# Optimization experiments

Measured on AMD Instinct MI355X. Metric: run time of the kernel, lower is better.

## Reference

```python
import jax, jax.numpy as jnp
import numpy as np

B, LC, LT = 2, 1024, 1024
DS, DF = 2, 1
EOBS = 4                 # nn.Embed(2, 4)
D_IN = EOBS + DS + DF    # concat(obs, s, f)
EMB_H, D = 256, 64       # embed_obs_s_f = MLP([256, 64])
H, DH = 8, 8             # heads x head_dim = D
FFN_H = 128              # ffn = MLP([128, 64])
BIAS_H = 16              # DistanceBias hidden width
HEAD_H = 128             # head = MLP([128, 2])
NBLK = 6                 # num_blks (num_reps = 1)
EPS = 1e-6

def _ln(x, scale, bias):
    mu = jnp.mean(x, -1, keepdims=True)
    var = jnp.var(x, -1, keepdims=True)
    return (x - mu) * jax.lax.rsqrt(var + EPS) * scale + bias

def _mlp(x, w1, b1, w2, b2):
    return jax.nn.relu(x @ w1 + b1) @ w2 + b2

def _dist_bias(d, w1, b1, w2, b2):
    # d: [B, Lq, Lk] scalar distances -> per-head bias [B, H, Lq, Lk]
    h = jax.nn.relu(d[..., None] @ w1 + b1)
    return jnp.transpose(h @ w2 + b2, (0, 3, 1, 2))

def _mha(q_in, kv_in, wq, bq, wk, bk, wv, bv, wo, bo, bias):
    q = (q_in @ wq + bq).reshape(*q_in.shape[:-1], H, DH)
    k = (kv_in @ wk + bk).reshape(*kv_in.shape[:-1], H, DH)
    v = (kv_in @ wv + bv).reshape(*kv_in.shape[:-1], H, DH)
    scores = jnp.einsum('bqhd,bkhd->bhqk', q, k) / np.sqrt(DH).astype(np.float32) + bias
    a = jax.nn.softmax(scores, axis=-1)
    o = jnp.einsum('bhqk,bkhd->bqhd', a, v).reshape(*q_in.shape[:-1], D)
    return o @ wo + bo

def _forward(s_ctx, f_ctx, s_test, embed_obs_table, emb_w1, emb_b1, emb_w2, emb_b2,
             attn_wq, attn_bq, attn_wk, attn_bk, attn_wv, attn_bv, attn_wo, attn_bo,
             ffn_w1, ffn_b1, ffn_w2, ffn_b2, bias_w1, bias_b1, bias_w2, bias_b2,
             norm_scale, norm_bias, fnorm_scale, fnorm_bias,
             head_w1, head_b1, head_w2, head_b2):
    Bv, Lt = s_test.shape[0], s_test.shape[1]
    f_test = jnp.zeros((Bv, Lt, f_ctx.shape[-1]), f_ctx.dtype)
    obs = jnp.broadcast_to(embed_obs_table[1], (*f_ctx.shape[:-1], EOBS))
    unobs = jnp.broadcast_to(embed_obs_table[0], (Bv, Lt, EOBS))
    kvs = _mlp(jnp.concatenate([obs, s_ctx, f_ctx], -1), emb_w1, emb_b1, emb_w2, emb_b2)
    qvs = _mlp(jnp.concatenate([unobs, s_test, f_test], -1), emb_w1, emb_b1, emb_w2, emb_b2)
    # vmap(l2_dist_sq): pairwise squared L2 distances per batch element
    d_qk = jnp.sum((s_test[:, :, None, :] - s_ctx[:, None, :, :]) ** 2, -1)
    d_kk = jnp.sum((s_ctx[:, :, None, :] - s_ctx[:, None, :, :]) ** 2, -1)
    for i in range(NBLK):
        b_qk = _dist_bias(d_qk, bias_w1[i], bias_b1[i], bias_w2[i], bias_b2[i])
        b_kk = _dist_bias(d_kk, bias_w1[i], bias_b1[i], bias_w2[i], bias_b2[i])
        aw = (attn_wq[i], attn_bq[i], attn_wk[i], attn_bk[i], attn_wv[i], attn_bv[i], attn_wo[i], attn_bo[i])
        ns, nb = norm_scale[i], norm_bias[i]
        q_att = _ln(qvs + _mha(qvs, kvs, *aw, b_qk), ns, nb)
        k_att = _ln(kvs + _mha(kvs, kvs, *aw, b_kk), ns, nb)
        qvs = _ln(q_att + _mlp(q_att, ffn_w1[i], ffn_b1[i], ffn_w2[i], ffn_b2[i]), ns, nb)
        kvs = _ln(k_att + _mlp(k_att, ffn_w1[i], ffn_b1[i], ffn_w2[i], ffn_b2[i]), ns, nb)
    qvs = _ln(qvs, fnorm_scale, fnorm_bias)
    f_dist = _mlp(qvs, head_w1, head_b1, head_w2, head_b2)
    f_mu, f_log_var = jnp.split(f_dist, 2, axis=-1)
    f_std = jnp.exp(f_log_var / 2)  # min_std = 0.0
    return f_mu, f_std

def setup_inputs() -> dict:
    key = jax.random.key(0)
    ks = iter(jax.random.split(key, 40))
    r = lambda shp, s=0.05: jax.random.normal(next(ks), shp, jnp.float32) * s
    return dict(
        s_ctx=r((B, LC, DS), 1.0), f_ctx=r((B, LC, DF), 1.0), s_test=r((B, LT, DS), 1.0),
        embed_obs_table=r((2, EOBS)),
        emb_w1=r((D_IN, EMB_H)), emb_b1=jnp.zeros((EMB_H,)),
        emb_w2=r((EMB_H, D)), emb_b2=jnp.zeros((D,)),
        attn_wq=r((NBLK, D, D)), attn_bq=jnp.zeros((NBLK, D)),
        attn_wk=r((NBLK, D, D)), attn_bk=jnp.zeros((NBLK, D)),
        attn_wv=r((NBLK, D, D)), attn_bv=jnp.zeros((NBLK, D)),
        attn_wo=r((NBLK, D, D)), attn_bo=jnp.zeros((NBLK, D)),
        ffn_w1=r((NBLK, D, FFN_H)), ffn_b1=jnp.zeros((NBLK, FFN_H)),
        ffn_w2=r((NBLK, FFN_H, D)), ffn_b2=jnp.zeros((NBLK, D)),
        bias_w1=r((NBLK, 1, BIAS_H)), bias_b1=jnp.zeros((NBLK, BIAS_H)),
        bias_w2=r((NBLK, BIAS_H, H)), bias_b2=jnp.zeros((NBLK, H)),
        norm_scale=jnp.ones((NBLK, D)), norm_bias=jnp.zeros((NBLK, D)),
        fnorm_scale=jnp.ones((D,)), fnorm_bias=jnp.zeros((D,)),
        head_w1=r((D, HEAD_H)), head_b1=jnp.zeros((HEAD_H,)),
        head_w2=r((HEAD_H, 2)), head_b2=jnp.zeros((2,)),
    )

def reference(s_ctx, f_ctx, s_test, embed_obs_table, emb_w1, emb_b1, emb_w2, emb_b2,
              attn_wq, attn_bq, attn_wk, attn_bk, attn_wv, attn_bv, attn_wo, attn_bo,
              ffn_w1, ffn_b1, ffn_w2, ffn_b2, bias_w1, bias_b1, bias_w2, bias_b2,
              norm_scale, norm_bias, fnorm_scale, fnorm_bias,
              head_w1, head_b1, head_w2, head_b2):
    return _forward(s_ctx, f_ctx, s_test, embed_obs_table, emb_w1, emb_b1, emb_w2, emb_b2,
                    attn_wq, attn_bq, attn_wk, attn_bk, attn_wv, attn_bv, attn_wo, attn_bo,
                    ffn_w1, ffn_b1, ffn_w2, ffn_b2, bias_w1, bias_b1, bias_w2, bias_b2,
                    norm_scale, norm_bias, fnorm_scale, fnorm_bias,
                    head_w1, head_b1, head_w2, head_b2)
```

## Files before the change

kernel.cpp:

```cpp
#include <hip/hip_runtime.h>
#include <hip/hip_bf16.h>

typedef __hip_bfloat16 bf16;
typedef float v2f __attribute__((ext_vector_type(2)));

#define LEN 1024
#define N2 2048
#define SCALE_L2E 0.5100697918f

#define I_SCTX   0
#define I_FCTX   4096
#define I_STEST  6144
#define I_OBS    10240
#define I_EW1    10248
#define I_EB1    12040
#define I_EW2    12296
#define I_EB2    28680
#define I_WQ     28744
#define I_BQ     53320
#define I_WK     53704
#define I_BK     78280
#define I_WV     78664
#define I_BV     103240
#define I_WO     103624
#define I_BO     128200
#define I_FW1    128584
#define I_FB1    177736
#define I_FW2    178504
#define I_FB2    227656
#define I_BW1    228040
#define I_BB1    228136
#define I_BW2    228232
#define I_BB2    229000
#define I_NS     229048
#define I_NB     229432
#define I_FNS    229816
#define I_FNB    229880
#define I_HW1    229944
#define I_HB1    238136
#define I_HW2    238264
#define I_HB2    238520

#define OFF_PW   240256
#define OFF_QVS  262144
#define OFF_KVS  393216
#define OFF_Q1   524288
#define OFF_Q2   655360
#define OFF_KB   786432
#define OFF_VB   917504
#define OFF_PART 1048576
#define PART_KS  196608

__constant__ int C_OFFS[33] = {
    0, 4096, 6144, 10240, 10248, 12040, 12296, 28680, 28744, 53320, 53704,
    78280, 78664, 103240, 103624, 128200, 128584, 177736, 178504, 227656,
    228040, 228136, 228232, 229000, 229048, 229432, 229816, 229880, 229944,
    238136, 238264, 238520, 238522 };

struct InPtrs { const void* p[32]; };

__device__ __forceinline__ float pack2(float a, float b) {
    __hip_bfloat16 ha = __float2bfloat16(a), hb = __float2bfloat16(b);
    unsigned ua = *(unsigned short*)&ha, ub = *(unsigned short*)&hb;
    return __uint_as_float(ua | (ub << 16));
}
__device__ __forceinline__ float unlo(float f) {
    return __uint_as_float(__float_as_uint(f) << 16);
}
__device__ __forceinline__ float unhi(float f) {
    return __uint_as_float(__float_as_uint(f) & 0xffff0000u);
}

__global__ __launch_bounds__(256) void k_cvt(InPtrs ptrs, float* ws) {
    const unsigned u0 = *(const unsigned*)ptrs.p[24];
    const int isbf = (u0 == 0x3F803F80u);
    const int i = blockIdx.y;
    const int o0 = C_OFFS[i], n = C_OFFS[i + 1] - o0;
    const void* src = ptrs.p[i];
    for (int j = blockIdx.x * 256 + threadIdx.x; j < n; j += gridDim.x * 256) {
        float v = isbf ? __bfloat162float(((const bf16*)src)[j])
                       : ((const float*)src)[j];
        ws[o0 + j] = v;
    }
}

__global__ __launch_bounds__(256) void k_pw(float* ws) {
    const int L = blockIdx.x, t = threadIdx.x;
    __shared__ float w1s[16], b1s[16], bps[16];
    __shared__ int rnk[16];
    if (t < 16) {
        float w = ws[I_BW1 + L * 16 + t], b0 = ws[I_BB1 + L * 16 + t];
        w1s[t] = w; b1s[t] = b0;
        bps[t] = (w != 0.f) ? (-b0 / w) : 1e30f;
    }
    __syncthreads();
    if (t < 16) {
        float me = bps[t]; int r = 0;
        for (int j = 0; j < 16; ++j) {
            float o = bps[j];
            if (o < me || (o == me && j < t)) ++r;
        }
        rnk[t] = r;
    }
    __syncthreads();
    if (t < 16) ws[OFF_PW + L * 288 + 272 + rnk[t]] = bps[t];
    if (t < 136) {
        int s = t >> 3, h = t & 7;
        float slope = 0.f, inter = ws[I_BB2 + L * 8 + h];
        for (int j = 0; j < 16; ++j) {
            float w = w1s[j];
            bool act = (w > 0.f) ? (rnk[j] < s)
                     : (w < 0.f) ? (rnk[j] >= s)
                                 : (b1s[j] > 0.f);
            if (act) {
                float w2v = ws[I_BW2 + L * 128 + j * 8 + h];
                slope += w * w2v;
                inter += b1s[j] * w2v;
            }
        }
        const float LOG2E = 1.4426950408889634f;
        ws[OFF_PW + L * 288 + (s * 8 + h) * 2]     = slope * LOG2E;
        ws[OFF_PW + L * 288 + (s * 8 + h) * 2 + 1] = inter * LOG2E;
    }
}

__global__ __launch_bounds__(256) void k_embed(float* ws) {
    __shared__ float hbuf[256];
    __shared__ float red[256];
    int r = blockIdx.x, t = threadIdx.x;
    bool is_ctx = (r < N2);
    int rr = is_ctx ? r : r - N2;
    const float* ob = ws + I_OBS + (is_ctx ? 4 : 0);
    const float* s  = ws + (is_ctx ? I_SCTX : I_STEST);
    float in[7];
    in[0] = ob[0]; in[1] = ob[1]; in[2] = ob[2]; in[3] = ob[3];
    in[4] = s[rr * 2]; in[5] = s[rr * 2 + 1];
    in[6] = is_ctx ? ws[I_FCTX + rr] : 0.f;

    float acc = ws[I_EB1 + t];
#pragma unroll
    for (int i = 0; i < 7; ++i) acc += in[i] * ws[I_EW1 + i * 256 + t];
    hbuf[t] = fmaxf(acc, 0.f);
    __syncthreads();

    int d = t & 63, p = t >> 6;
    float a2 = 0.f;
#pragma unroll 8
    for (int j = p * 64; j < p * 64 + 64; ++j) a2 += hbuf[j] * ws[I_EW2 + j * 64 + d];
    red[t] = a2;
    __syncthreads();
    if (t < 64) {
        float o = red[t] + red[64 + t] + red[128 + t] + red[192 + t] + ws[I_EB2 + t];
        float* dst = ws + (is_ctx ? OFF_KVS : OFF_QVS);
        dst[rr * 64 + t] = o;
    }
}

__global__ __launch_bounds__(256) void k_qkv(int blk, float* ws) {
    __shared__ float xs[2][64];
    int r = blockIdx.x, t = threadIdx.x;
    if (t < 64)       xs[0][t] = ws[OFF_QVS + r * 64 + t];
    else if (t < 128) xs[1][t - 64] = ws[OFF_KVS + r * 64 + (t - 64)];
    __syncthreads();
    int o = t >> 6, d = t & 63;
    const float* x = (o == 0) ? xs[0] : xs[1];
    const float* W; const float* bb; float* dst;
    if (o <= 1)      { W = ws + I_WQ + blk * 4096; bb = ws + I_BQ + blk * 64; dst = ws + (o == 0 ? OFF_Q1 : OFF_Q2); }
    else if (o == 2) { W = ws + I_WK + blk * 4096; bb = ws + I_BK + blk * 64; dst = ws + OFF_KB; }
    else             { W = ws + I_WV + blk * 4096; bb = ws + I_BV + blk * 64; dst = ws + OFF_VB; }
    float acc = bb[d];
#pragma unroll 8
    for (int k = 0; k < 64; ++k) acc += x[k] * W[k * 64 + d];
    dst[r * 64 + d] = acc;
}

__global__ __launch_bounds__(256, 4) void k_attn(int blk, float* ws) {
    __shared__ float Ks[2176];
    __shared__ float Vs[2176];
    __shared__ float Sds[544];
    __shared__ v2f   pw[136];

    const int t = threadIdx.x;
    const int qt = blockIdx.x, ks = blockIdx.y, z = blockIdx.z;
    const int b = z & 1, kind = z >> 1;
    const int q0 = qt * 16;
    const float* Qbuf = ws + (kind == 0 ? OFF_Q1 : OFF_Q2);
    const float* Kbuf = ws + OFF_KB;
    const float* Vbuf = ws + OFF_VB;
    const float* sq_src = ws + (kind == 0 ? I_STEST : I_SCTX);
    const float* sk_src = ws + I_SCTX;
    const float* pwg = ws + OFF_PW + blk * 288;

    float bp[16];
#pragma unroll
    for (int j = 0; j < 16; ++j) bp[j] = pwg[272 + j];

    if (t < 136) pw[t] = (v2f){ pwg[t * 2], pwg[t * 2 + 1] };

    const int par = t & 7, h2 = (t >> 3) & 7, q4 = t >> 6;
    const int pq = t >> 4, pk = t & 15;
    float sqx, sqy;
    {
        const float* sp = sq_src + (b * LEN + q0 + pq) * 2;
        sqx = sp[0]; sqy = sp[1];
    }

    v2f qf[4][4];
#pragma unroll
    for (int i = 0; i < 4; ++i) {
        const float* qp = Qbuf + (b * LEN + q0 + q4 + 4 * i) * 64 + h2 * 8;
        float4 qa = *(const float4*)qp;
        float4 qb = *(const float4*)(qp + 4);
        qf[i][0] = (v2f){qa.x, qa.y}; qf[i][1] = (v2f){qa.z, qa.w};
        qf[i][2] = (v2f){qb.x, qb.y}; qf[i][3] = (v2f){qb.z, qb.w};
    }

    float m[4] = {-1e30f, -1e30f, -1e30f, -1e30f};
    float l[4] = {};
    v2f oacc[4][4] = {};

    for (int kt = ks * 4; kt < ks * 4 + 4; ++kt) {
        __syncthreads();
        {
            int kr = t >> 3, j = (t & 7) * 8;
            const float* ksrc = Kbuf + (b * LEN + kt * 32 + kr) * 64 + j;
            const float* vsrc = Vbuf + (b * LEN + kt * 32 + kr) * 64 + j;
            *(float4*)&Ks[kr * 68 + j]     = *(const float4*)ksrc;
            *(float4*)&Ks[kr * 68 + j + 4] = *(const float4*)(ksrc + 4);
            *(float4*)&Vs[kr * 68 + j]     = *(const float4*)vsrc;
            *(float4*)&Vs[kr * 68 + j + 4] = *(const float4*)(vsrc + 4);
        }
        {
            float4 kc = *(const float4*)(sk_src + (b * LEN + kt * 32 + pk * 2) * 2);
            float dx0 = sqx - kc.x, dy0 = sqy - kc.y;
            float dx1 = sqx - kc.z, dy1 = sqy - kc.w;
            float d0 = dx0 * dx0 + dy0 * dy0;
            float d1 = dx1 * dx1 + dy1 * dy1;
            int s0 = 0, s1 = 0;
#pragma unroll
            for (int j = 0; j < 16; ++j) { s0 += (d0 > bp[j]); s1 += (d1 > bp[j]); }
            Sds[(pk * 2) * 17 + pq]     = __uint_as_float((__float_as_uint(d0) & ~31u) | s0);
            Sds[(pk * 2 + 1) * 17 + pq] = __uint_as_float((__float_as_uint(d1) & ~31u) | s1);
        }
        __syncthreads();

        float sv[16];
#pragma unroll
        for (int j = 0; j < 4; ++j) {
            int k = par + 8 * j;
            const v2f* kf = (const v2f*)&Ks[k * 68 + h2 * 8];
            v2f k0 = kf[0], k1 = kf[1], k2 = kf[2], k3 = kf[3];
#pragma unroll
            for (int i = 0; i < 4; ++i) {
                unsigned u = __float_as_uint(Sds[k * 17 + q4 + 4 * i]);
                float dv = __uint_as_float(u & ~31u);
                v2f pv_ = pw[(u & 31u) * 8 + h2];
                v2f acc = qf[i][0] * k0;
                acc += qf[i][1] * k1;
                acc += qf[i][2] * k2;
                acc += qf[i][3] * k3;
                sv[i * 4 + j] = (acc.x + acc.y) * SCALE_L2E + (pv_.x * dv + pv_.y);
            }
        }
#pragma unroll
        for (int i = 0; i < 4; ++i) {
            float tm = m[i];
#pragma unroll
            for (int j = 0; j < 4; ++j) tm = fmaxf(tm, sv[i * 4 + j]);
            float alpha = exp2f(m[i] - tm);
            l[i] *= alpha;
            v2f av = (v2f){alpha, alpha};
#pragma unroll
            for (int c = 0; c < 4; ++c) oacc[i][c] *= av;
            m[i] = tm;
#pragma unroll
            for (int j = 0; j < 4; ++j) {
                float p = exp2f(sv[i * 4 + j] - tm);
                sv[i * 4 + j] = p;
                l[i] += p;
            }
        }
#pragma unroll
        for (int j = 0; j < 4; ++j) {
            int k = par + 8 * j;
            const v2f* vf = (const v2f*)&Vs[k * 68 + h2 * 8];
            v2f v0 = vf[0], v1 = vf[1], v2 = vf[2], v3 = vf[3];
#pragma unroll
            for (int i = 0; i < 4; ++i) {
                float p = sv[i * 4 + j];
                v2f pp = (v2f){p, p};
                oacc[i][0] += pp * v0;
                oacc[i][1] += pp * v1;
                oacc[i][2] += pp * v2;
                oacc[i][3] += pp * v3;
            }
        }
    }

#pragma unroll
    for (int st = 1; st <= 4; st <<= 1) {
#pragma unroll
        for (int i = 0; i < 4; ++i) {
            float mo = __shfl_xor(m[i], st);
            float Mx = fmaxf(m[i], mo);
            float a0 = exp2f(m[i] - Mx), a1 = exp2f(mo - Mx);
            float lo = __shfl_xor(l[i], st);
            l[i] = l[i] * a0 + lo * a1;
#pragma unroll
            for (int c = 0; c < 4; ++c) {
                v2f x = oacc[i][c];
                float x0 = x.x * a0 + __shfl_xor(x.x, st) * a1;
                float x1 = x.y * a0 + __shfl_xor(x.y, st) * a1;
                oacc[i][c] = (v2f){x0, x1};
            }
            m[i] = Mx;
        }
    }

    __syncthreads();
    float* stg = Ks;
    if (par == 0) {
#pragma unroll
        for (int i = 0; i < 4; ++i) {
            float inv = 1.f / l[i];
            float lse = m[i] + log2f(l[i]);
            float* p = &stg[(q4 + 4 * i) * 48 + h2 * 6];
            p[0] = pack2(oacc[i][0].x * inv, oacc[i][0].y * inv);
            p[1] = pack2(oacc[i][1].x * inv, oacc[i][1].y * inv);
            p[2] = pack2(oacc[i][2].x * inv, oacc[i][2].y * inv);
            p[3] = pack2(oacc[i][3].x * inv, oacc[i][3].y * inv);
            p[4] = lse; p[5] = 0.f;
        }
    }
    __syncthreads();
    if (t < 192) {
        float* dst = ws + OFF_PART + ks * PART_KS + (z * LEN + q0) * 48;
        *(float4*)(dst + t * 4) = *(const float4*)(stg + t * 4);
    }
}

__global__ __launch_bounds__(128) void k_fuse(int blk, float* ws, const void* ns_raw, void* out_raw) {
    __shared__ float xo[4 * 68];
    __shared__ float xsm[4 * 68];
    __shared__ float hs[4 * 132];
    __shared__ float xn[4 * 68];
    const int t = threadIdx.x;
    const int kind = blockIdx.y;
    const int r0 = blockIdx.x * 4;
    float* io = ws + (kind == 0 ? OFF_QVS : OFF_KVS);

    {
        int r = t >> 5, h = (t >> 2) & 7, q = t & 3;
        int rg = r0 + r, b = rg >> 10, row = rg & 1023, z = kind * 2 + b;
        const float* e0 = ws + OFF_PART + q * PART_KS + ((z * LEN + row) * 8 + h) * 6;
        const float* e1 = e0 + 4 * PART_KS;
        v2f a0 = *(const v2f*)e0, a1 = *(const v2f*)(e0 + 2), a2 = *(const v2f*)(e0 + 4);
        v2f c0 = *(const v2f*)e1, c1 = *(const v2f*)(e1 + 2), c2 = *(const v2f*)(e1 + 4);
        float M = fmaxf(a2.x, c2.x);
        M = fmaxf(M, __shfl_xor(M, 1));
        M = fmaxf(M, __shfl_xor(M, 2));
        float wA = exp2f(a2.x - M), wB = exp2f(c2.x - M);
        float den = wA + wB;
        float num[8];
        num[0] = wA * unlo(a0.x) + wB * unlo(c0.x);
        num[1] = wA * unhi(a0.x) + wB * unhi(c0.x);
        num[2] = wA * unlo(a0.y) + wB * unlo(c0.y);
        num[3] = wA * unhi(a0.y) + wB * unhi(c0.y);
        num[4] = wA * unlo(a1.x) + wB * unlo(c1.x);
        num[5] = wA * unhi(a1.x) + wB * unhi(c1.x);
        num[6] = wA * unlo(a1.y) + wB * unlo(c1.y);
        num[7] = wA * unhi(a1.y) + wB * unhi(c1.y);
        den += __shfl_xor(den, 1); den += __shfl_xor(den, 2);
#pragma unroll
        for (int d_ = 0; d_ < 8; ++d_) {
            num[d_] += __shfl_xor(num[d_], 1);
            num[d_] += __shfl_xor(num[d_], 2);
        }
        float invd = 1.f / den;
        xo[r * 68 + h * 8 + 2 * q]     = num[2 * q] * invd;
        xo[r * 68 + h * 8 + 2 * q + 1] = num[2 * q + 1] * invd;
    }
    __syncthreads();

    const int r = t >> 5, dd = (t & 31) * 2;
    const int rg = r0 + r;
    float xs0, xs1;

    {
        const float* Wo = ws + I_WO + blk * 4096;
        v2f acc = *(const v2f*)(ws + I_BO + blk * 64 + dd);
#pragma unroll 8
        for (int k = 0; k < 64; ++k) {
            float xv = xo[r * 68 + k];
            v2f w = *(const v2f*)(Wo + k * 64 + dd);
            acc.x += xv * w.x; acc.y += xv * w.y;
        }
        v2f rv = *(const v2f*)(io + rg * 64 + dd);
        acc.x += rv.x; acc.y += rv.y;
        float s = acc.x + acc.y, s2 = acc.x * acc.x + acc.y * acc.y;
#pragma unroll
        for (int off = 1; off < 32; off <<= 1) { s += __shfl_xor(s, off); s2 += __shfl_xor(s2, off); }
        float mu = s * (1.f / 64.f);
        float var = s2 * (1.f / 64.f) - mu * mu;
        float rs = rsqrtf(fmaxf(var, 0.f) + 1e-6f);
        v2f nsv = *(const v2f*)(ws + I_NS + blk * 64 + dd);
        v2f nbv = *(const v2f*)(ws + I_NB + blk * 64 + dd);
        xs0 = (acc.x - mu) * rs * nsv.x + nbv.x;
        xs1 = (acc.y - mu) * rs * nsv.y + nbv.y;
        *(v2f*)&xsm[r * 68 + dd] = (v2f){xs0, xs1};
    }
    __syncthreads();

    {
        int rc = t >> 5, c4 = (t & 31) * 4;
        const float* W1 = ws + I_FW1 + blk * 8192;
        float4 acc = *(const float4*)(ws + I_FB1 + blk * 128 + c4);
#pragma unroll 4
        for (int k = 0; k < 64; ++k) {
            float xv = xsm[rc * 68 + k];
            float4 w = *(const float4*)(W1 + k * 128 + c4);
            acc.x += xv * w.x; acc.y += xv * w.y; acc.z += xv * w.z; acc.w += xv * w.w;
        }
        acc.x = fmaxf(acc.x, 0.f); acc.y = fmaxf(acc.y, 0.f);
        acc.z = fmaxf(acc.z, 0.f); acc.w = fmaxf(acc.w, 0.f);
        *(float4*)&hs[rc * 132 + c4] = acc;
    }
    __syncthreads();

    float v0, v1;
    {
        const float* W2 = ws + I_FW2 + blk * 8192;
        v2f acc = *(const v2f*)(ws + I_FB2 + blk * 64 + dd);
#pragma unroll 8
        for (int k = 0; k < 128; ++k) {
            float hv = hs[r * 132 + k];
            v2f w = *(const v2f*)(W2 + k * 64 + dd);
            acc.x += hv * w.x; acc.y += hv * w.y;
        }
        acc.x += xs0; acc.y += xs1;
        float s = acc.x + acc.y, s2 = acc.x * acc.x + acc.y * acc.y;
#pragma unroll
        for (int off = 1; off < 32; off <<= 1) { s += __shfl_xor(s, off); s2 += __shfl_xor(s2, off); }
        float mu = s * (1.f / 64.f);
        float var = s2 * (1.f / 64.f) - mu * mu;
        float rs = rsqrtf(fmaxf(var, 0.f) + 1e-6f);
        v2f nsv = *(const v2f*)(ws + I_NS + blk * 64 + dd);
        v2f nbv = *(const v2f*)(ws + I_NB + blk * 64 + dd);
        v0 = (acc.x - mu) * rs * nsv.x + nbv.x;
        v1 = (acc.y - mu) * rs * nsv.y + nbv.y;
        *(v2f*)(io + rg * 64 + dd) = (v2f){v0, v1};
        *(v2f*)&xn[r * 68 + dd] = (v2f){v0, v1};
    }
    __syncthreads();

    if (blk < 5) {
        const int nb_ = blk + 1;
        if (kind == 0) {
            const float* WQ = ws + I_WQ + nb_ * 4096;
            v2f acc = *(const v2f*)(ws + I_BQ + nb_ * 64 + dd);
#pragma unroll 8
            for (int k = 0; k < 64; ++k) {
                float xv = xn[r * 68 + k];
                v2f w = *(const v2f*)(WQ + k * 64 + dd);
                acc.x += xv * w.x; acc.y += xv * w.y;
            }
            *(v2f*)(ws + OFF_Q1 + rg * 64 + dd) = acc;
        } else {
            const float* WQ = ws + I_WQ + nb_ * 4096;
            const float* WK = ws + I_WK + nb_ * 4096;
            const float* WV = ws + I_WV + nb_ * 4096;
            v2f aq = *(const v2f*)(ws + I_BQ + nb_ * 64 + dd);
            v2f ak = *(const v2f*)(ws + I_BK + nb_ * 64 + dd);
            v2f av = *(const v2f*)(ws + I_BV + nb_ * 64 + dd);
#pragma unroll 4
            for (int k = 0; k < 64; ++k) {
                float xv = xn[r * 68 + k];
                v2f wq = *(const v2f*)(WQ + k * 64 + dd);
                v2f wk = *(const v2f*)(WK + k * 64 + dd);
                v2f wv = *(const v2f*)(WV + k * 64 + dd);
                aq.x += xv * wq.x; aq.y += xv * wq.y;
                ak.x += xv * wk.x; ak.y += xv * wk.y;
                av.x += xv * wv.x; av.y += xv * wv.y;
            }
            *(v2f*)(ws + OFF_Q2 + rg * 64 + dd) = aq;
            *(v2f*)(ws + OFF_KB + rg * 64 + dd) = ak;
            *(v2f*)(ws + OFF_VB + rg * 64 + dd) = av;
        }
    } else if (kind == 0) {
        {
            float s = v0 + v1, s2 = v0 * v0 + v1 * v1;
#pragma unroll
            for (int off = 1; off < 32; off <<= 1) { s += __shfl_xor(s, off); s2 += __shfl_xor(s2, off); }
            float mu = s * (1.f / 64.f);
            float var = s2 * (1.f / 64.f) - mu * mu;
            float rs = rsqrtf(fmaxf(var, 0.f) + 1e-6f);
            v2f fns = *(const v2f*)(ws + I_FNS + dd);
            v2f fnb = *(const v2f*)(ws + I_FNB + dd);
            *(v2f*)&xsm[r * 68 + dd] = (v2f){ (v0 - mu) * rs * fns.x + fnb.x,
                                              (v1 - mu) * rs * fns.y + fnb.y };
        }
        __syncthreads();
        {
            int rc = t >> 5, c4 = (t & 31) * 4;
            const float* W1 = ws + I_HW1;
            float4 acc = *(const float4*)(ws + I_HB1 + c4);
#pragma unroll 4
            for (int k = 0; k < 64; ++k) {
                float xv = xsm[rc * 68 + k];
                float4 w = *(const float4*)(W1 + k * 128 + c4);
                acc.x += xv * w.x; acc.y += xv * w.y; acc.z += xv * w.z; acc.w += xv * w.w;
            }
            acc.x = fmaxf(acc.x, 0.f); acc.y = fmaxf(acc.y, 0.f);
            acc.z = fmaxf(acc.z, 0.f); acc.w = fmaxf(acc.w, 0.f);
            *(float4*)&hs[rc * 132 + c4] = acc;
        }
        __syncthreads();
        if (t < 8) {
            int rr = t >> 1, c = t & 1;
            float a = ws[I_HB2 + c];
            for (int k = 0; k < 128; ++k) a += hs[rr * 132 + k] * ws[I_HW2 + k * 2 + c];
            float v = c ? exp2f(a * 0.7213475204444817f) : a;
            int rgg = r0 + rr;
            int idx = c ? (N2 + rgg) : rgg;
            unsigned u0 = *(const unsigned*)ns_raw;
            if (u0 == 0x3F803F80u) ((bf16*)out_raw)[idx] = __float2bfloat16(v);
            else                   ((float*)out_raw)[idx] = v;
        }
    }
}

extern "C" void kernel_launch(void* const* d_in, const int* in_sizes, int n_in,
                              void* d_out, int out_size, void* d_ws, size_t ws_size,
                              hipStream_t stream) {
    float* ws = (float*)d_ws;

    InPtrs ptrs;
    for (int i = 0; i < 32; ++i) ptrs.p[i] = d_in[i];

    k_cvt<<<dim3(8, 32), 256, 0, stream>>>(ptrs, ws);
    k_pw<<<6, 256, 0, stream>>>(ws);
    k_embed<<<4096, 256, 0, stream>>>(ws);
    k_qkv<<<2048, 256, 0, stream>>>(0, ws);
    for (int i = 0; i < 6; ++i) {
        k_attn<<<dim3(64, 8, 4), 256, 0, stream>>>(i, ws);
        k_fuse<<<dim3(512, 2), 128, 0, stream>>>(i, ws, d_in[24], d_out);
    }
}
```

Measured before the change: 634.3 us.

## Shrink attention per-thread tiles, write partials directly, and split fuse into 2-row blocks

k_attn now gives each thread 2 query rows and 8 keys instead of 4 rows and 4 keys, which cuts register use so launch bounds can rise to 7 waves per SIMD. Partial outputs go straight to global memory in a per-row, per-head layout, removing the shared-memory staging and its barrier. k_fuse becomes a 64-thread block handling 2 rows, with twice as many blocks, and merges all 8 key-split partials per head inside one thread instead of shuffling. The trade-offs are more scattered small global writes from attention, more softmax merge steps per output, and more redundant weight reads across the smaller fuse blocks.

```diff
diff --git a/kernel.cpp b/kernel.cpp
--- a/kernel.cpp
+++ b/kernel.cpp
@@ -49,7 +49,6 @@
 #define OFF_KB   786432
 #define OFF_VB   917504
 #define OFF_PART 1048576
-#define PART_KS  196608
 
 __constant__ int C_OFFS[33] = {
     0, 4096, 6144, 10240, 10248, 12040, 12296, 28680, 28744, 53320, 53704,
@@ -174,7 +173,7 @@
     dst[r * 64 + d] = acc;
 }
 
-__global__ __launch_bounds__(256, 4) void k_attn(int blk, float* ws) {
+__global__ __launch_bounds__(256, 7) void k_attn(int blk, float* ws) {
     __shared__ float Ks[2176];
     __shared__ float Vs[2176];
     __shared__ float Sds[544];
@@ -197,7 +196,7 @@
 
     if (t < 136) pw[t] = (v2f){ pwg[t * 2], pwg[t * 2 + 1] };
 
-    const int par = t & 7, h2 = (t >> 3) & 7, q4 = t >> 6;
+    const int q2 = t >> 5, h2 = (t >> 2) & 7, par = t & 3;
     const int pq = t >> 4, pk = t & 15;
     float sqx, sqy;
     {
@@ -205,19 +204,19 @@
         sqx = sp[0]; sqy = sp[1];
     }
 
-    v2f qf[4][4];
-#pragma unroll
-    for (int i = 0; i < 4; ++i) {
-        const float* qp = Qbuf + (b * LEN + q0 + q4 + 4 * i) * 64 + h2 * 8;
+    v2f qf[2][4];
+#pragma unroll
+    for (int i = 0; i < 2; ++i) {
+        const float* qp = Qbuf + (b * LEN + q0 + q2 + 8 * i) * 64 + h2 * 8;
         float4 qa = *(const float4*)qp;
         float4 qb = *(const float4*)(qp + 4);
         qf[i][0] = (v2f){qa.x, qa.y}; qf[i][1] = (v2f){qa.z, qa.w};
         qf[i][2] = (v2f){qb.x, qb.y}; qf[i][3] = (v2f){qb.z, qb.w};
     }
 
-    float m[4] = {-1e30f, -1e30f, -1e30f, -1e30f};
-    float l[4] = {};
-    v2f oacc[4][4] = {};
+    float m[2] = {-1e30f, -1e30f};
+    float l[2] = {};
+    v2f oacc[2][4] = {};
 
     for (int kt = ks * 4; kt < ks * 4 + 4; ++kt) {
         __syncthreads();
@@ -244,29 +243,29 @@
         }
         __syncthreads();
 
-        float sv[16];
-#pragma unroll
-        for (int j = 0; j < 4; ++j) {
-            int k = par + 8 * j;
+        float sv[2][8];
+#pragma unroll
+        for (int j = 0; j < 8; ++j) {
+            int k = par + 4 * j;
             const v2f* kf = (const v2f*)&Ks[k * 68 + h2 * 8];
             v2f k0 = kf[0], k1 = kf[1], k2 = kf[2], k3 = kf[3];
 #pragma unroll
-            for (int i = 0; i < 4; ++i) {
-                unsigned u = __float_as_uint(Sds[k * 17 + q4 + 4 * i]);
+            for (int i = 0; i < 2; ++i) {
+                unsigned u = __float_as_uint(Sds[k * 17 + q2 + 8 * i]);
                 float dv = __uint_as_float(u & ~31u);
                 v2f pv_ = pw[(u & 31u) * 8 + h2];
                 v2f acc = qf[i][0] * k0;
                 acc += qf[i][1] * k1;
                 acc += qf[i][2] * k2;
                 acc += qf[i][3] * k3;
-                sv[i * 4 + j] = (acc.x + acc.y) * SCALE_L2E + (pv_.x * dv + pv_.y);
-            }
-        }
-#pragma unroll
-        for (int i = 0; i < 4; ++i) {
+                sv[i][j] = (acc.x + acc.y) * SCALE_L2E + (pv_.x * dv + pv_.y);
+            }
+        }
+#pragma unroll
+        for (int i = 0; i < 2; ++i) {
             float tm = m[i];
 #pragma unroll
-            for (int j = 0; j < 4; ++j) tm = fmaxf(tm, sv[i * 4 + j]);
+            for (int j = 0; j < 8; ++j) tm = fmaxf(tm, sv[i][j]);
             float alpha = exp2f(m[i] - tm);
             l[i] *= alpha;
             v2f av = (v2f){alpha, alpha};
@@ -274,20 +273,20 @@
             for (int c = 0; c < 4; ++c) oacc[i][c] *= av;
             m[i] = tm;
 #pragma unroll
-            for (int j = 0; j < 4; ++j) {
-                float p = exp2f(sv[i * 4 + j] - tm);
-                sv[i * 4 + j] = p;
+            for (int j = 0; j < 8; ++j) {
+                float p = exp2f(sv[i][j] - tm);
+                sv[i][j] = p;
                 l[i] += p;
             }
         }
 #pragma unroll
-        for (int j = 0; j < 4; ++j) {
-            int k = par + 8 * j;
+        for (int j = 0; j < 8; ++j) {
+            int k = par + 4 * j;
             const v2f* vf = (const v2f*)&Vs[k * 68 + h2 * 8];
             v2f v0 = vf[0], v1 = vf[1], v2 = vf[2], v3 = vf[3];
 #pragma unroll
-            for (int i = 0; i < 4; ++i) {
-                float p = sv[i * 4 + j];
+            for (int i = 0; i < 2; ++i) {
+                float p = sv[i][j];
                 v2f pp = (v2f){p, p};
                 oacc[i][0] += pp * v0;
                 oacc[i][1] += pp * v1;
@@ -298,9 +297,9 @@
     }
 
 #pragma unroll
-    for (int st = 1; st <= 4; st <<= 1) {
-#pragma unroll
-        for (int i = 0; i < 4; ++i) {
+    for (int st = 1; st <= 2; st <<= 1) {
+#pragma unroll
+        for (int i = 0; i < 2; ++i) {
             float mo = __shfl_xor(m[i], st);
             float Mx = fmaxf(m[i], mo);
             float a0 = exp2f(m[i] - Mx), a1 = exp2f(mo - Mx);
@@ -317,139 +316,131 @@
         }
     }
 
-    __syncthreads();
-    float* stg = Ks;
     if (par == 0) {
 #pragma unroll
-        for (int i = 0; i < 4; ++i) {
+        for (int i = 0; i < 2; ++i) {
             float inv = 1.f / l[i];
             float lse = m[i] + log2f(l[i]);
-            float* p = &stg[(q4 + 4 * i) * 48 + h2 * 6];
-            p[0] = pack2(oacc[i][0].x * inv, oacc[i][0].y * inv);
-            p[1] = pack2(oacc[i][1].x * inv, oacc[i][1].y * inv);
-            p[2] = pack2(oacc[i][2].x * inv, oacc[i][2].y * inv);
-            p[3] = pack2(oacc[i][3].x * inv, oacc[i][3].y * inv);
-            p[4] = lse; p[5] = 0.f;
-        }
-    }
-    __syncthreads();
-    if (t < 192) {
-        float* dst = ws + OFF_PART + ks * PART_KS + (z * LEN + q0) * 48;
-        *(float4*)(dst + t * 4) = *(const float4*)(stg + t * 4);
-    }
-}
-
-__global__ __launch_bounds__(128) void k_fuse(int blk, float* ws, const void* ns_raw, void* out_raw) {
-    __shared__ float xo[4 * 68];
-    __shared__ float xsm[4 * 68];
-    __shared__ float hs[4 * 132];
-    __shared__ float xn[4 * 68];
+            int row = q0 + q2 + 8 * i;
+            float* p = ws + OFF_PART + (z * LEN + row) * 384 + h2 * 48 + ks * 6;
+            *(v2f*)(p)     = (v2f){ pack2(oacc[i][0].x * inv, oacc[i][0].y * inv),
+                                    pack2(oacc[i][1].x * inv, oacc[i][1].y * inv) };
+            *(v2f*)(p + 2) = (v2f){ pack2(oacc[i][2].x * inv, oacc[i][2].y * inv),
+                                    pack2(oacc[i][3].x * inv, oacc[i][3].y * inv) };
+            *(v2f*)(p + 4) = (v2f){ lse, 0.f };
+        }
+    }
+}
+
+__global__ __launch_bounds__(64) void k_fuse(int blk, float* ws, const void* ns_raw, void* out_raw) {
+    __shared__ float xo[2][64];
+    __shared__ float xsm[2][64];
+    __shared__ float hs[2][128];
+    __shared__ float xn[2][64];
     const int t = threadIdx.x;
     const int kind = blockIdx.y;
-    const int r0 = blockIdx.x * 4;
+    const int g = blockIdx.x;
+    const int rg0 = g * 2, rg1 = g * 2 + 1;
     float* io = ws + (kind == 0 ? OFF_QVS : OFF_KVS);
 
     {
-        int r = t >> 5, h = (t >> 2) & 7, q = t & 3;
-        int rg = r0 + r, b = rg >> 10, row = rg & 1023, z = kind * 2 + b;
-        const float* e0 = ws + OFF_PART + q * PART_KS + ((z * LEN + row) * 8 + h) * 6;
-        const float* e1 = e0 + 4 * PART_KS;
-        v2f a0 = *(const v2f*)e0, a1 = *(const v2f*)(e0 + 2), a2 = *(const v2f*)(e0 + 4);
-        v2f c0 = *(const v2f*)e1, c1 = *(const v2f*)(e1 + 2), c2 = *(const v2f*)(e1 + 4);
-        float M = fmaxf(a2.x, c2.x);
-        M = fmaxf(M, __shfl_xor(M, 1));
-        M = fmaxf(M, __shfl_xor(M, 2));
-        float wA = exp2f(a2.x - M), wB = exp2f(c2.x - M);
-        float den = wA + wB;
-        float num[8];
-        num[0] = wA * unlo(a0.x) + wB * unlo(c0.x);
-        num[1] = wA * unhi(a0.x) + wB * unhi(c0.x);
-        num[2] = wA * unlo(a0.y) + wB * unlo(c0.y);
-        num[3] = wA * unhi(a0.y) + wB * unhi(c0.y);
-        num[4] = wA * unlo(a1.x) + wB * unlo(c1.x);
-        num[5] = wA * unhi(a1.x) + wB * unhi(c1.x);
-        num[6] = wA * unlo(a1.y) + wB * unlo(c1.y);
-        num[7] = wA * unhi(a1.y) + wB * unhi(c1.y);
-        den += __shfl_xor(den, 1); den += __shfl_xor(den, 2);
-#pragma unroll
-        for (int d_ = 0; d_ < 8; ++d_) {
-            num[d_] += __shfl_xor(num[d_], 1);
-            num[d_] += __shfl_xor(num[d_], 2);
-        }
-        float invd = 1.f / den;
-        xo[r * 68 + h * 8 + 2 * q]     = num[2 * q] * invd;
-        xo[r * 68 + h * 8 + 2 * q + 1] = num[2 * q + 1] * invd;
-    }
-    __syncthreads();
-
-    const int r = t >> 5, dd = (t & 31) * 2;
-    const int rg = r0 + r;
+        int h = t >> 3, d = t & 7;
+#pragma unroll
+        for (int r = 0; r < 2; ++r) {
+            int rg = g * 2 + r, b = rg >> 10, row = rg & 1023, z = kind * 2 + b;
+            const float* base = ws + OFF_PART + (z * LEN + row) * 384 + h * 48;
+            float ls[8];
+            float M = -1e30f;
+#pragma unroll
+            for (int k2 = 0; k2 < 8; ++k2) { ls[k2] = base[k2 * 6 + 4]; M = fmaxf(M, ls[k2]); }
+            float den = 0.f, num = 0.f;
+#pragma unroll
+            for (int k2 = 0; k2 < 8; ++k2) {
+                float e = exp2f(ls[k2] - M);
+                den += e;
+                float pf = base[k2 * 6 + (d >> 1)];
+                float o = (d & 1) ? unhi(pf) : unlo(pf);
+                num += e * o;
+            }
+            xo[r][h * 8 + d] = num / den;
+        }
+    }
+    __syncthreads();
+
     float xs0, xs1;
-
     {
         const float* Wo = ws + I_WO + blk * 4096;
-        v2f acc = *(const v2f*)(ws + I_BO + blk * 64 + dd);
+        float bo = ws[I_BO + blk * 64 + t];
+        float a0 = bo, a1 = bo;
 #pragma unroll 8
         for (int k = 0; k < 64; ++k) {
-            float xv = xo[r * 68 + k];
-            v2f w = *(const v2f*)(Wo + k * 64 + dd);
-            acc.x += xv * w.x; acc.y += xv * w.y;
-        }
-        v2f rv = *(const v2f*)(io + rg * 64 + dd);
-        acc.x += rv.x; acc.y += rv.y;
-        float s = acc.x + acc.y, s2 = acc.x * acc.x + acc.y * acc.y;
-#pragma unroll
-        for (int off = 1; off < 32; off <<= 1) { s += __shfl_xor(s, off); s2 += __shfl_xor(s2, off); }
-        float mu = s * (1.f / 64.f);
-        float var = s2 * (1.f / 64.f) - mu * mu;
-        float rs = rsqrtf(fmaxf(var, 0.f) + 1e-6f);
-        v2f nsv = *(const v2f*)(ws + I_NS + blk * 64 + dd);
-        v2f nbv = *(const v2f*)(ws + I_NB + blk * 64 + dd);
-        xs0 = (acc.x - mu) * rs * nsv.x + nbv.x;
-        xs1 = (acc.y - mu) * rs * nsv.y + nbv.y;
-        *(v2f*)&xsm[r * 68 + dd] = (v2f){xs0, xs1};
+            float w = Wo[k * 64 + t];
+            a0 += xo[0][k] * w;
+            a1 += xo[1][k] * w;
+        }
+        a0 += io[rg0 * 64 + t];
+        a1 += io[rg1 * 64 + t];
+        float s0 = a0, q0_ = a0 * a0, s1 = a1, q1_ = a1 * a1;
+#pragma unroll
+        for (int off = 1; off < 64; off <<= 1) {
+            s0 += __shfl_xor(s0, off); q0_ += __shfl_xor(q0_, off);
+            s1 += __shfl_xor(s1, off); q1_ += __shfl_xor(q1_, off);
+        }
+        float mu0 = s0 * (1.f / 64.f), var0 = q0_ * (1.f / 64.f) - mu0 * mu0;
+        float mu1 = s1 * (1.f / 64.f), var1 = q1_ * (1.f / 64.f) - mu1 * mu1;
+        float rs0 = rsqrtf(fmaxf(var0, 0.f) + 1e-6f);
+        float rs1 = rsqrtf(fmaxf(var1, 0.f) + 1e-6f);
+        float nsv = ws[I_NS + blk * 64 + t], nbv = ws[I_NB + blk * 64 + t];
+        xs0 = (a0 - mu0) * rs0 * nsv + nbv;
+        xs1 = (a1 - mu1) * rs1 * nsv + nbv;
+        xsm[0][t] = xs0; xsm[1][t] = xs1;
     }
     __syncthreads();
 
     {
-        int rc = t >> 5, c4 = (t & 31) * 4;
         const float* W1 = ws + I_FW1 + blk * 8192;
-        float4 acc = *(const float4*)(ws + I_FB1 + blk * 128 + c4);
-#pragma unroll 4
+        float b0 = ws[I_FB1 + blk * 128 + t], b1 = ws[I_FB1 + blk * 128 + t + 64];
+        float a00 = b0, a01 = b1, a10 = b0, a11 = b1;
+#pragma unroll 8
         for (int k = 0; k < 64; ++k) {
-            float xv = xsm[rc * 68 + k];
-            float4 w = *(const float4*)(W1 + k * 128 + c4);
-            acc.x += xv * w.x; acc.y += xv * w.y; acc.z += xv * w.z; acc.w += xv * w.w;
-        }
-        acc.x = fmaxf(acc.x, 0.f); acc.y = fmaxf(acc.y, 0.f);
-        acc.z = fmaxf(acc.z, 0.f); acc.w = fmaxf(acc.w, 0.f);
-        *(float4*)&hs[rc * 132 + c4] = acc;
-    }
-    __syncthreads();
-
-    float v0, v1;
+            float w0 = W1[k * 128 + t], w1 = W1[k * 128 + t + 64];
+            float x0 = xsm[0][k], x1 = xsm[1][k];
+            a00 += x0 * w0; a01 += x0 * w1;
+            a10 += x1 * w0; a11 += x1 * w1;
+        }
+        hs[0][t] = fmaxf(a00, 0.f); hs[0][t + 64] = fmaxf(a01, 0.f);
+        hs[1][t] = fmaxf(a10, 0.f); hs[1][t + 64] = fmaxf(a11, 0.f);
+    }
+    __syncthreads();
+
+    float v00, v10;
     {
         const float* W2 = ws + I_FW2 + blk * 8192;
-        v2f acc = *(const v2f*)(ws + I_FB2 + blk * 64 + dd);
+        float b2 = ws[I_FB2 + blk * 64 + t];
+        float a0 = b2, a1 = b2;
 #pragma unroll 8
         for (int k = 0; k < 128; ++k) {
-            float hv = hs[r * 132 + k];
-            v2f w = *(const v2f*)(W2 + k * 64 + dd);
-            acc.x += hv * w.x; acc.y += hv * w.y;
-        }
-        acc.x += xs0; acc.y += xs1;
-        float s = acc.x + acc.y, s2 = acc.x * acc.x + acc.y * acc.y;
-#pragma unroll
-        for (int off = 1; off < 32; off <<= 1) { s += __shfl_xor(s, off); s2 += __shfl_xor(s2, off); }
-        float mu = s * (1.f / 64.f);
-        float var = s2 * (1.f / 64.f) - mu * mu;
-        float rs = rsqrtf(fmaxf(var, 0.f) + 1e-6f);
-        v2f nsv = *(const v2f*)(ws + I_NS + blk * 64 + dd);
-        v2f nbv = *(const v2f*)(ws + I_NB + blk * 64 + dd);
-        v0 = (acc.x - mu) * rs * nsv.x + nbv.x;
-        v1 = (acc.y - mu) * rs * nsv.y + nbv.y;
-        *(v2f*)(io + rg * 64 + dd) = (v2f){v0, v1};
-        *(v2f*)&xn[r * 68 + dd] = (v2f){v0, v1};
+            float w = W2[k * 64 + t];
+            a0 += hs[0][k] * w;
+            a1 += hs[1][k] * w;
+        }
+        a0 += xs0; a1 += xs1;
+        float s0 = a0, q0_ = a0 * a0, s1 = a1, q1_ = a1 * a1;
+#pragma unroll
+        for (int off = 1; off < 64; off <<= 1) {
+            s0 += __shfl_xor(s0, off); q0_ += __shfl_xor(q0_, off);
+            s1 += __shfl_xor(s1, off); q1_ += __shfl_xor(q1_, off);
+        }
+        float mu0 = s0 * (1.f / 64.f), var0 = q0_ * (1.f / 64.f) - mu0 * mu0;
+        float mu1 = s1 * (1.f / 64.f), var1 = q1_ * (1.f / 64.f) - mu1 * mu1;
+        float rs0 = rsqrtf(fmaxf(var0, 0.f) + 1e-6f);
+        float rs1 = rsqrtf(fmaxf(var1, 0.f) + 1e-6f);
+        float nsv = ws[I_NS + blk * 64 + t], nbv = ws[I_NB + blk * 64 + t];
+        v00 = (a0 - mu0) * rs0 * nsv + nbv;
+        v10 = (a1 - mu1) * rs1 * nsv + nbv;
+        io[rg0 * 64 + t] = v00;
+        io[rg1 * 64 + t] = v10;
+        xn[0][t] = v00; xn[1][t] = v10;
     }
     __syncthreads();
 
@@ -457,70 +448,74 @@
         const int nb_ = blk + 1;
         if (kind == 0) {
             const float* WQ = ws + I_WQ + nb_ * 4096;
-            v2f acc = *(const v2f*)(ws + I_BQ + nb_ * 64 + dd);
+            float bq = ws[I_BQ + nb_ * 64 + t];
+            float a0 = bq, a1 = bq;
 #pragma unroll 8
             for (int k = 0; k < 64; ++k) {
-                float xv = xn[r * 68 + k];
-                v2f w = *(const v2f*)(WQ + k * 64 + dd);
-                acc.x += xv * w.x; acc.y += xv * w.y;
-            }
-            *(v2f*)(ws + OFF_Q1 + rg * 64 + dd) = acc;
+                float w = WQ[k * 64 + t];
+                a0 += xn[0][k] * w;
+                a1 += xn[1][k] * w;
+            }
+            ws[OFF_Q1 + rg0 * 64 + t] = a0;
+            ws[OFF_Q1 + rg1 * 64 + t] = a1;
         } else {
             const float* WQ = ws + I_WQ + nb_ * 4096;
             const float* WK = ws + I_WK + nb_ * 4096;
             const float* WV = ws + I_WV + nb_ * 4096;
-            v2f aq = *(const v2f*)(ws + I_BQ + nb_ * 64 + dd);
-            v2f ak = *(const v2f*)(ws + I_BK + nb_ * 64 + dd);
-            v2f av = *(const v2f*)(ws + I_BV + nb_ * 64 + dd);
+            float bq = ws[I_BQ + nb_ * 64 + t];
+            float bk = ws[I_BK + nb_ * 64 + t];
+            float bv = ws[I_BV + nb_ * 64 + t];
+            float q0a = bq, q1a = bq, k0a = bk, k1a = bk, v0a = bv, v1a = bv;
 #pragma unroll 4
             for (int k = 0; k < 64; ++k) {
-                float xv = xn[r * 68 + k];
-                v2f wq = *(const v2f*)(WQ + k * 64 + dd);
-                v2f wk = *(const v2f*)(WK + k * 64 + dd);
-                v2f wv = *(const v2f*)(WV + k * 64 + dd);
-                aq.x += xv * wq.x; aq.y += xv * wq.y;
-                ak.x += xv * wk.x; ak.y += xv * wk.y;
-                av.x += xv * wv.x; av.y += xv * wv.y;
-            }
-            *(v2f*)(ws + OFF_Q2 + rg * 64 + dd) = aq;
-            *(v2f*)(ws + OFF_KB + rg * 64 + dd) = ak;
-            *(v2f*)(ws + OFF_VB + rg * 64 + dd) = av;
+                float wq = WQ[k * 64 + t], wk = WK[k * 64 + t], wv = WV[k * 64 + t];
+                float x0 = xn[0][k], x1 = xn[1][k];
+                q0a += x0 * wq; q1a += x1 * wq;
+                k0a += x0 * wk; k1a += x1 * wk;
+                v0a += x0 * wv; v1a += x1 * wv;
+            }
+            ws[OFF_Q2 + rg0 * 64 + t] = q0a; ws[OFF_Q2 + rg1 * 64 + t] = q1a;
+            ws[OFF_KB + rg0 * 64 + t] = k0a; ws[OFF_KB + rg1 * 64 + t] = k1a;
+            ws[OFF_VB + rg0 * 64 + t] = v0a; ws[OFF_VB + rg1 * 64 + t] = v1a;
         }
     } else if (kind == 0) {
         {
-            float s = v0 + v1, s2 = v0 * v0 + v1 * v1;
-#pragma unroll
-            for (int off = 1; off < 32; off <<= 1) { s += __shfl_xor(s, off); s2 += __shfl_xor(s2, off); }
-            float mu = s * (1.f / 64.f);
-            float var = s2 * (1.f / 64.f) - mu * mu;
-            float rs = rsqrtf(fmaxf(var, 0.f) + 1e-6f);
-            v2f fns = *(const v2f*)(ws + I_FNS + dd);
-            v2f fnb = *(const v2f*)(ws + I_FNB + dd);
-            *(v2f*)&xsm[r * 68 + dd] = (v2f){ (v0 - mu) * rs * fns.x + fnb.x,
-                                              (v1 - mu) * rs * fns.y + fnb.y };
+            float s0 = v00, q0_ = v00 * v00, s1 = v10, q1_ = v10 * v10;
+#pragma unroll
+            for (int off = 1; off < 64; off <<= 1) {
+                s0 += __shfl_xor(s0, off); q0_ += __shfl_xor(q0_, off);
+                s1 += __shfl_xor(s1, off); q1_ += __shfl_xor(q1_, off);
+            }
+            float mu0 = s0 * (1.f / 64.f), var0 = q0_ * (1.f / 64.f) - mu0 * mu0;
+            float mu1 = s1 * (1.f / 64.f), var1 = q1_ * (1.f / 64.f) - mu1 * mu1;
+            float rs0 = rsqrtf(fmaxf(var0, 0.f) + 1e-6f);
+            float rs1 = rsqrtf(fmaxf(var1, 0.f) + 1e-6f);
+            float fns = ws[I_FNS + t], fnb = ws[I_FNB + t];
+            xsm[0][t] = (v00 - mu0) * rs0 * fns + fnb;
+            xsm[1][t] = (v10 - mu1) * rs1 * fns + fnb;
         }
         __syncthreads();
         {
-            int rc = t >> 5, c4 = (t & 31) * 4;
             const float* W1 = ws + I_HW1;
-            float4 acc = *(const float4*)(ws + I_HB1 + c4);
-#pragma unroll 4
+            float b0 = ws[I_HB1 + t], b1 = ws[I_HB1 + t + 64];
+            float a00 = b0, a01 = b1, a10 = b0, a11 = b1;
+#pragma unroll 8
             for (int k = 0; k < 64; ++k) {
-                float xv = xsm[rc * 68 + k];
-                float4 w = *(const float4*)(W1 + k * 128 + c4);
-                acc.x += xv * w.x; acc.y += xv * w.y; acc.z += xv * w.z; acc.w += xv * w.w;
-            }
-            acc.x = fmaxf(acc.x, 0.f); acc.y = fmaxf(acc.y, 0.f);
-            acc.z = fmaxf(acc.z, 0.f); acc.w = fmaxf(acc.w, 0.f);
-            *(float4*)&hs[rc * 132 + c4] = acc;
+                float w0 = W1[k * 128 + t], w1 = W1[k * 128 + t + 64];
+                float x0 = xsm[0][k], x1 = xsm[1][k];
+                a00 += x0 * w0; a01 += x0 * w1;
+                a10 += x1 * w0; a11 += x1 * w1;
+            }
+            hs[0][t] = fmaxf(a00, 0.f); hs[0][t + 64] = fmaxf(a01, 0.f);
+            hs[1][t] = fmaxf(a10, 0.f); hs[1][t + 64] = fmaxf(a11, 0.f);
         }
         __syncthreads();
-        if (t < 8) {
+        if (t < 4) {
             int rr = t >> 1, c = t & 1;
             float a = ws[I_HB2 + c];
-            for (int k = 0; k < 128; ++k) a += hs[rr * 132 + k] * ws[I_HW2 + k * 2 + c];
+            for (int k = 0; k < 128; ++k) a += hs[rr][k] * ws[I_HW2 + k * 2 + c];
             float v = c ? exp2f(a * 0.7213475204444817f) : a;
-            int rgg = r0 + rr;
+            int rgg = g * 2 + rr;
             int idx = c ? (N2 + rgg) : rgg;
             unsigned u0 = *(const unsigned*)ns_raw;
             if (u0 == 0x3F803F80u) ((bf16*)out_raw)[idx] = __float2bfloat16(v);
@@ -543,6 +538,6 @@
     k_qkv<<<2048, 256, 0, stream>>>(0, ws);
     for (int i = 0; i < 6; ++i) {
         k_attn<<<dim3(64, 8, 4), 256, 0, stream>>>(i, ws);
-        k_fuse<<<dim3(512, 2), 128, 0, stream>>>(i, ws, d_in[24], d_out);
-    }
-}
+        k_fuse<<<dim3(1024, 2), 64, 0, stream>>>(i, ws, d_in[24], d_out);
+    }
+}
```

Measured after the change: 712.6 us. +12.3%, slower.
